# Kernel tuning notes

Measured on AMD Instinct MI355X. Metric: run time of the kernel, lower is better.

## Reference

```python
import jax, jax.numpy as jnp
import numpy as np

H = 8
D_MODEL = 512
D_K = D_MODEL // H
B = 8
S = 1024


def _linear(x, W, b):
    # torch nn.Linear: y = x @ W.T + b, W: [out, in]
    return jnp.einsum('bsd,ed->bse', x, W) + b


def _to_heads(x):
    # [B,S,D] -> [B,H,S,d_k]
    return x.reshape(B, S, H, D_K).transpose(0, 2, 1, 3)


def setup_inputs() -> dict:
    key = jax.random.key(0)
    ks = jax.random.split(key, 20)
    inp = {
        'input_rgb': jax.random.normal(ks[0], (B, S, D_MODEL), jnp.float32),
        'input_flow': jax.random.normal(ks[1], (B, S, D_MODEL), jnp.float32),
    }
    names = ['Wq1', 'Wk1', 'Wv1', 'Wq2', 'Wk2', 'Wv2', 'Wo1', 'Wo2']
    for i, n in enumerate(names):
        inp[n] = jax.random.normal(ks[2 + i], (D_MODEL, D_MODEL), jnp.float32) * 0.02
        inp['b' + n[1:]] = jax.random.normal(ks[10 + i], (D_MODEL,), jnp.float32) * 0.02
    return inp


def reference(input_rgb, input_flow, Wq1, bq1, Wk1, bk1, Wv1, bv1,
              Wq2, bq2, Wk2, bk2, Wv2, bv2, Wo1, bo1, Wo2, bo2):
    scale = 1.0 / jnp.sqrt(jnp.asarray(D_K, input_rgb.dtype))

    q_r = _to_heads(_linear(input_rgb, Wq1, bq1))
    k_r = _to_heads(_linear(input_rgb, Wk1, bk1))
    v_r = _to_heads(_linear(input_rgb, Wv1, bv1))
    q_f = _to_heads(_linear(input_flow, Wq2, bq2))
    k_f = _to_heads(_linear(input_flow, Wk2, bk2))
    v_f = _to_heads(_linear(input_flow, Wv2, bv2))

    # two full [B,H,S,S] softmax attention maps
    attn_rgb = jax.nn.softmax(jnp.einsum('bhqd,bhkd->bhqk', q_r, k_r) * scale, axis=-1)
    attn_flow = jax.nn.softmax(jnp.einsum('bhqd,bhkd->bhqk', q_f, k_f) * scale, axis=-1)
    # elementwise max merge (breaks flash-attention fusion)
    attn = jnp.maximum(attn_rgb, attn_flow)

    # Attention2: out = attn @ value (dropout is identity in eval mode)
    out_rgb = jnp.einsum('bhqk,bhkd->bhqd', attn, v_r)
    out_flow = jnp.einsum('bhqk,bhkd->bhqd', attn, v_f)

    out_rgb = out_rgb.transpose(0, 2, 1, 3).reshape(B, S, D_MODEL)
    out_flow = out_flow.transpose(0, 2, 1, 3).reshape(B, S, D_MODEL)
    return (_linear(out_rgb, Wo1, bo1), _linear(out_flow, Wo2, bo2))
```

## Files before the change

### kernel.cpp

```cpp
#include <hip/hip_runtime.h>
#include <hip/hip_bf16.h>


typedef unsigned short u16;
typedef __attribute__((ext_vector_type(8))) short short8;
typedef __attribute__((ext_vector_type(4))) short s4pack;
typedef __attribute__((ext_vector_type(4))) float floatx4;

#define B_DIM 8
#define S_DIM 1024
#define H_DIM 8
#define DK 64
#define DMODEL 512
#define NTOK (B_DIM * S_DIM)
#define SEG ((size_t)NTOK * DMODEL)
#define WSEG ((size_t)DMODEL * DMODEL)

#define SCHED_FENCE() __builtin_amdgcn_sched_barrier(0)
#define LGKM0() asm volatile("s_waitcnt lgkmcnt(0)" ::: "memory")
#define BARRIER() __builtin_amdgcn_s_barrier()

__device__ __forceinline__ floatx4 mfma_bf16(short8 a, short8 b, floatx4 c) {
  return __builtin_amdgcn_mfma_f32_16x16x32_bf16(a, b, c, 0, 0, 0);
}

__device__ __forceinline__ u16 f32_to_bf16_rne(float f) {
  unsigned u = __float_as_uint(f);
  unsigned r = u + 0x7FFFu + ((u >> 16) & 1u);
  return (u16)(r >> 16);
}

__device__ __forceinline__ float bf16_bits_to_f32(u16 u) {
  return __uint_as_float(((unsigned)u) << 16);
}

__device__ __forceinline__ void async_cp16(const u16* g, u16* lds) {
  __builtin_amdgcn_global_load_lds(
      (__attribute__((address_space(1))) void*)(const_cast<u16*>(g)),
      (__attribute__((address_space(3))) void*)(lds), 16, 0, 0);
}

#define NT_CONV 18
#define CCHUNK 8192
struct ConvParams {
  const void* src[NT_CONV];
  u16* dst[NT_CONV];
  int n[NT_CONV];
  int coff[NT_CONV + 1];
};

__global__ __launch_bounds__(256) void convert_inputs(ConvParams p) {
  __shared__ int flag_f32;
  const int blk = blockIdx.x;
  int t = 0;
  while (t + 1 < NT_CONV && blk >= p.coff[t + 1]) ++t;
  const int lc = blk - p.coff[t];
  const int n = p.n[t];
  const int tid = threadIdx.x;

  if (tid < 64) {
    const u16* s = (const u16*)p.src[t];
    int bad = 0;
#pragma unroll
    for (int j = 0; j < 8; ++j) {
      float f = bf16_bits_to_f32(s[tid * 8 + j]);
      bad |= !(fabsf(f) < 1e4f);
    }
    bad |= __shfl_xor(bad, 1);
    bad |= __shfl_xor(bad, 2);
    bad |= __shfl_xor(bad, 4);
    bad |= __shfl_xor(bad, 8);
    bad |= __shfl_xor(bad, 16);
    bad |= __shfl_xor(bad, 32);
    if (tid == 0) flag_f32 = bad;
  }
  __syncthreads();
  const int is_f32 = flag_f32;
  const int base = lc * CCHUNK;

#pragma unroll
  for (int it = 0; it < CCHUNK / 2048; ++it) {
    const int idx = base + (it * 256 + tid) * 8;
    if (idx + 8 > n) break;
    if (!is_f32) {
      *(short8*)&p.dst[t][idx] = *(const short8*)&((const u16*)p.src[t])[idx];
    } else {
      const float* s = (const float*)p.src[t] + idx;
      short8 o;
#pragma unroll
      for (int j = 0; j < 8; ++j) o[j] = (short)f32_to_bf16_rne(s[j]);
      *(short8*)&p.dst[t][idx] = o;
    }
  }
}

__device__ __forceinline__ void gemm128_mainloop(
    const u16* __restrict__ A, const u16* __restrict__ W,
    int m0, int n0, u16* ldsA, u16* ldsB, floatx4 acc[4][4]) {
  const int tid = threadIdx.x;
  const int lane = tid & 63;
  const int wid = tid >> 6;
  const int wm = wid >> 1, wn = wid & 1;
  const int r = lane & 15, g = lane >> 4;

  const int stg_row = wid * 32 + (lane >> 2);
  const int stg_col = (((lane & 3) ^ ((lane >> 3) & 3)) * 8);

  const u16* ga0 = A + (size_t)(m0 + stg_row) * DMODEL + stg_col;
  const u16* ga1 = A + (size_t)(m0 + stg_row + 16) * DMODEL + stg_col;
  const u16* gb0 = W + (size_t)(n0 + stg_row) * DMODEL + stg_col;
  const u16* gb1 = W + (size_t)(n0 + stg_row + 16) * DMODEL + stg_col;
  const int lo0 = (wid * 32) * 32;
  const int lo1 = (wid * 32 + 16) * 32;

#pragma unroll
  for (int t = 0; t < 3; ++t) {
    const int nb = t * 4096;
    const int ko = t * 32;
    async_cp16(ga0 + ko, ldsA + nb + lo0);
    async_cp16(ga1 + ko, ldsA + nb + lo1);
    async_cp16(gb0 + ko, ldsB + nb + lo0);
    async_cp16(gb1 + ko, ldsB + nb + lo1);
  }

  const int rc = ((g ^ ((r >> 1) & 3)) * 8);

#pragma unroll
  for (int kt = 0; kt < 16; ++kt) {
    SCHED_FENCE();
    if (kt < 14)       asm volatile("s_waitcnt vmcnt(8)" ::: "memory");
    else if (kt == 14) asm volatile("s_waitcnt vmcnt(4)" ::: "memory");
    else               asm volatile("s_waitcnt vmcnt(0)" ::: "memory");
    BARRIER();
    SCHED_FENCE();

    const int cb = (kt % 3) * 4096;
    short8 a[4], b[4];
#pragma unroll
    for (int i = 0; i < 4; ++i)
      a[i] = *(const short8*)&ldsA[cb + (wm * 64 + i * 16 + r) * 32 + rc];
#pragma unroll
    for (int j = 0; j < 4; ++j)
      b[j] = *(const short8*)&ldsB[cb + (wn * 64 + j * 16 + r) * 32 + rc];
#pragma unroll
    for (int i = 0; i < 4; ++i)
#pragma unroll
      for (int j = 0; j < 4; ++j)
        acc[i][j] = mfma_bf16(a[i], b[j], acc[i][j]);

    if (kt + 3 < 16) {
      SCHED_FENCE(); BARRIER(); SCHED_FENCE();
      const int ko = (kt + 3) * 32;
      async_cp16(ga0 + ko, ldsA + cb + lo0);
      async_cp16(ga1 + ko, ldsA + cb + lo1);
      async_cp16(gb0 + ko, ldsB + cb + lo0);
      async_cp16(gb1 + ko, ldsB + cb + lo1);
    }
  }
}

struct QkvParams {
  const u16* X[2];
  const u16* W[2][3];
  const u16* Bias[2][3];
  u16* Out[2][3];
};

__global__ __launch_bounds__(256) void qkv_gemm(QkvParams p) {
  __shared__ u16 ldsA[3 * 128 * 32];
  __shared__ u16 ldsB[3 * 128 * 32];
  const int lin = blockIdx.x;
  const int wg = (lin & 7) * 192 + (lin >> 3);
  const int m0 = (wg / 24) * 128;
  const int c = wg % 24;
  const int z = c / 12;
  const int yc = c % 12;
  const int wi = yc >> 2;
  const int n0 = (yc & 3) * 128;

  floatx4 acc[4][4];
  const floatx4 z4 = {0.f, 0.f, 0.f, 0.f};
#pragma unroll
  for (int i = 0; i < 4; ++i)
#pragma unroll
    for (int j = 0; j < 4; ++j) acc[i][j] = z4;

  gemm128_mainloop(p.X[z], p.W[z][wi], m0, n0, ldsA, ldsB, acc);

  const int tid = threadIdx.x, lane = tid & 63, wid = tid >> 6;
  const int wm = wid >> 1, wn = wid & 1, r = lane & 15, g = lane >> 4;
  const u16* bias = p.Bias[z][wi];
  u16* out = p.Out[z][wi];
  const float qscale = 0.125f * 1.4426950408889634f;

#pragma unroll
  for (int j = 0; j < 4; ++j) {
    const int cc = n0 + wn * 64 + j * 16 + r;
    const float bv = bf16_bits_to_f32(bias[cc]);
    const int h = cc >> 6, d = cc & 63;
#pragma unroll
    for (int i = 0; i < 4; ++i) {
      const int row0 = m0 + wm * 64 + i * 16 + g * 4;
      const int bb = row0 >> 10, ss0 = row0 & 1023;
      if (wi == 2) {
        s4pack pk;
#pragma unroll
        for (int ii = 0; ii < 4; ++ii)
          pk[ii] = (short)f32_to_bf16_rne(acc[i][j][ii] + bv);
        *(s4pack*)&out[(((size_t)(bb * H_DIM + h)) * DK + d) * S_DIM + ss0] = pk;
      } else {
#pragma unroll
        for (int ii = 0; ii < 4; ++ii) {
          float v = acc[i][j][ii] + bv;
          if (wi == 0) v *= qscale;
          out[(((size_t)(bb * H_DIM + h)) * S_DIM + (ss0 + ii)) * DK + d] =
              f32_to_bf16_rne(v);
        }
      }
    }
  }
}

#define KVB 64
#define QB 128

struct AttnParams {
  const u16* Q[2];
  const u16* K[2];
  const u16* Vt[2];
  u16* O[2];
};

__global__ __launch_bounds__(256, 2) void attn_merged(AttnParams p) {
  __shared__ u16 Ks[2][KVB * 64];
  __shared__ u16 Vs[2][64 * KVB];

  const int tid = threadIdx.x;
  const int lane = tid & 63;
  const int wid = tid >> 6;
  const int r = lane & 15, g = lane >> 4;

  const int lin = blockIdx.x;
  const int w = (lin & 7) * 64 + (lin >> 3);
  const int bh = w >> 3;
  const int q0 = (w & 7) * QB;
  const size_t hbase = (size_t)bh * S_DIM * DK;

  const int krow = tid >> 3, kch = tid & 7;
  const int sK = (krow & 3) | (((krow >> 3) & 1) << 2);
  const int kdst0 = krow * 64 + ((kch ^ sK) * 8);
  const int kdst1 = (krow + 32) * 64 + ((kch ^ sK) * 8);
  const size_t kg0 = (size_t)krow * DK + kch * 8;
  const size_t kg1 = kg0 + (size_t)32 * DK;

  const int vrow = tid >> 3, vch = tid & 7;
  const int sV = vrow & 7;
  const int vdst0 = vrow * KVB + ((vch ^ sV) * 8);
  const int vdst1 = (vrow + 32) * KVB + ((vch ^ sV) * 8);
  const size_t vg0 = (size_t)vrow * S_DIM + vch * 8;
  const size_t vg1 = vg0 + (size_t)32 * S_DIM;

  const int srg = (r & 3) | (((r >> 2) & 1) << 2);
  const int prow = ((r >> 2) * 8 + (r & 3)) * 64;
  const int cA0 = (g ^ srg) * 8;
  const int cA1 = ((4 + g) ^ srg) * 8;

  short8 qf[2][2][2];
#pragma unroll
  for (int s = 0; s < 2; ++s)
#pragma unroll
    for (int mt = 0; mt < 2; ++mt)
#pragma unroll
      for (int kc = 0; kc < 2; ++kc)
        qf[s][mt][kc] = *(const short8*)
            &p.Q[s][hbase + (size_t)(q0 + wid * 32 + mt * 16 + r) * DK +
                    kc * 32 + g * 8];

  short8 kst[2][2], vst[2][2];
#pragma unroll
  for (int s = 0; s < 2; ++s) {
    kst[s][0] = *(const short8*)&p.K[s][hbase + kg0];
    kst[s][1] = *(const short8*)&p.K[s][hbase + kg1];
  }

  const floatx4 z4 = {0.f, 0.f, 0.f, 0.f};
  float sl[2][2] = {{0.f, 0.f}, {0.f, 0.f}};

  for (int kt = 0; kt < 16; ++kt) {
    if (kt) { SCHED_FENCE(); BARRIER(); SCHED_FENCE(); }
#pragma unroll
    for (int s = 0; s < 2; ++s) {
      *(short8*)&Ks[s][kdst0] = kst[s][0];
      *(short8*)&Ks[s][kdst1] = kst[s][1];
    }
    if (kt < 15) {
      const size_t k0n = (size_t)(kt + 1) * KVB * DK;
#pragma unroll
      for (int s = 0; s < 2; ++s) {
        kst[s][0] = *(const short8*)&p.K[s][hbase + k0n + kg0];
        kst[s][1] = *(const short8*)&p.K[s][hbase + k0n + kg1];
      }
    }
    SCHED_FENCE(); LGKM0(); BARRIER(); SCHED_FENCE();

#pragma unroll
    for (int kb = 0; kb < 2; ++kb) {
      const int ro = kb * 2048 + prow;
#pragma unroll
      for (int s = 0; s < 2; ++s) {
        const short8 kA0 = *(const short8*)&Ks[s][ro + cA0];
        const short8 kA1 = *(const short8*)&Ks[s][ro + cA1];
        const short8 kB0 = *(const short8*)&Ks[s][ro + 256 + cA0];
        const short8 kB1 = *(const short8*)&Ks[s][ro + 256 + cA1];
#pragma unroll
        for (int mt = 0; mt < 2; ++mt) {
          floatx4 aA = mfma_bf16(kA0, qf[s][mt][0], z4);
          aA = mfma_bf16(kA1, qf[s][mt][1], aA);
          floatx4 aB = mfma_bf16(kB0, qf[s][mt][0], z4);
          aB = mfma_bf16(kB1, qf[s][mt][1], aB);
          sl[s][mt] += __builtin_amdgcn_exp2f(aA[0]) + __builtin_amdgcn_exp2f(aA[1]) +
                       __builtin_amdgcn_exp2f(aA[2]) + __builtin_amdgcn_exp2f(aA[3]) +
                       __builtin_amdgcn_exp2f(aB[0]) + __builtin_amdgcn_exp2f(aB[1]) +
                       __builtin_amdgcn_exp2f(aB[2]) + __builtin_amdgcn_exp2f(aB[3]);
        }
      }
    }
  }

#pragma unroll
  for (int s = 0; s < 2; ++s) {
    kst[s][0] = *(const short8*)&p.K[s][hbase + kg0];
    kst[s][1] = *(const short8*)&p.K[s][hbase + kg1];
    vst[s][0] = *(const short8*)&p.Vt[s][hbase + vg0];
    vst[s][1] = *(const short8*)&p.Vt[s][hbase + vg1];
  }

  float inv_[2][2];
#pragma unroll
  for (int s = 0; s < 2; ++s)
#pragma unroll
    for (int mt = 0; mt < 2; ++mt) {
      float v = sl[s][mt];
      v += __shfl_xor(v, 16);
      v += __shfl_xor(v, 32);
      inv_[s][mt] = 1.0f / v;
    }

  floatx4 o_[2][2][4];
#pragma unroll
  for (int s = 0; s < 2; ++s)
#pragma unroll
    for (int mt = 0; mt < 2; ++mt)
#pragma unroll
      for (int nt = 0; nt < 4; ++nt) o_[s][mt][nt] = z4;

  for (int kt = 0; kt < 16; ++kt) {
    SCHED_FENCE(); BARRIER(); SCHED_FENCE();
#pragma unroll
    for (int s = 0; s < 2; ++s) {
      *(short8*)&Ks[s][kdst0] = kst[s][0];
      *(short8*)&Ks[s][kdst1] = kst[s][1];
      *(short8*)&Vs[s][vdst0] = vst[s][0];
      *(short8*)&Vs[s][vdst1] = vst[s][1];
    }
    if (kt < 15) {
      const size_t knk = (size_t)(kt + 1) * KVB;
#pragma unroll
      for (int s = 0; s < 2; ++s) {
        kst[s][0] = *(const short8*)&p.K[s][hbase + knk * DK + kg0];
        kst[s][1] = *(const short8*)&p.K[s][hbase + knk * DK + kg1];
        vst[s][0] = *(const short8*)&p.Vt[s][hbase + vg0 + knk];
        vst[s][1] = *(const short8*)&p.Vt[s][hbase + vg1 + knk];
      }
    }
    SCHED_FENCE(); LGKM0(); BARRIER(); SCHED_FENCE();

#pragma unroll
    for (int kb = 0; kb < 2; ++kb) {
      const int ro = kb * 2048 + prow;
      short8 kA0[2], kA1[2], kB0[2], kB1[2];
#pragma unroll
      for (int s = 0; s < 2; ++s) {
        kA0[s] = *(const short8*)&Ks[s][ro + cA0];
        kA1[s] = *(const short8*)&Ks[s][ro + cA1];
        kB0[s] = *(const short8*)&Ks[s][ro + 256 + cA0];
        kB1[s] = *(const short8*)&Ks[s][ro + 256 + cA1];
      }

      short8 pA[2];
#pragma unroll
      for (int mt = 0; mt < 2; ++mt) {
        floatx4 arA = mfma_bf16(kA0[0], qf[0][mt][0], z4);
        arA = mfma_bf16(kA1[0], qf[0][mt][1], arA);
        floatx4 arB = mfma_bf16(kB0[0], qf[0][mt][0], z4);
        arB = mfma_bf16(kB1[0], qf[0][mt][1], arB);
        floatx4 afA = mfma_bf16(kA0[1], qf[1][mt][0], z4);
        afA = mfma_bf16(kA1[1], qf[1][mt][1], afA);
        floatx4 afB = mfma_bf16(kB0[1], qf[1][mt][0], z4);
        afB = mfma_bf16(kB1[1], qf[1][mt][1], afB);
#pragma unroll
        for (int i = 0; i < 4; ++i) {
          const float prA = __builtin_amdgcn_exp2f(arA[i]) * inv_[0][mt];
          const float pfA = __builtin_amdgcn_exp2f(afA[i]) * inv_[1][mt];
          pA[mt][i] = (short)f32_to_bf16_rne(fmaxf(prA, pfA));
          const float prB = __builtin_amdgcn_exp2f(arB[i]) * inv_[0][mt];
          const float pfB = __builtin_amdgcn_exp2f(afB[i]) * inv_[1][mt];
          pA[mt][4 + i] = (short)f32_to_bf16_rne(fmaxf(prB, pfB));
        }
      }

      short8 vB[2][4];
#pragma unroll
      for (int s = 0; s < 2; ++s)
#pragma unroll
        for (int nt = 0; nt < 4; ++nt)
          vB[s][nt] = *(const short8*)
              &Vs[s][(nt * 16 + r) * KVB + (((kb * 4 + g) ^ (r & 7)) * 8)];

#pragma unroll
      for (int s = 0; s < 2; ++s)
#pragma unroll
        for (int mt = 0; mt < 2; ++mt)
#pragma unroll
          for (int nt = 0; nt < 4; ++nt)
            o_[s][mt][nt] = mfma_bf16(pA[mt], vB[s][nt], o_[s][mt][nt]);
    }
  }

  const int bb = bh >> 3, h = bh & 7;
#pragma unroll
  for (int s = 0; s < 2; ++s) {
    u16* out = p.O[s];
#pragma unroll
    for (int mt = 0; mt < 2; ++mt)
#pragma unroll
      for (int nt = 0; nt < 4; ++nt) {
        const int col = h * 64 + nt * 16 + r;
#pragma unroll
        for (int i = 0; i < 4; ++i) {
          const int row = q0 + wid * 32 + mt * 16 + g * 4 + i;
          out[((size_t)bb * S_DIM + row) * DMODEL + col] =
              f32_to_bf16_rne(o_[s][mt][nt][i]);
        }
      }
  }
}

struct OutParams {
  const u16* A[2];
  const u16* W[2];
  const u16* Bias[2];
  float* Out[2];
};

__global__ __launch_bounds__(256) void out_gemm(OutParams p) {
  __shared__ u16 ldsA[3 * 128 * 32];
  __shared__ u16 ldsB[3 * 128 * 32];
  const int lin = blockIdx.x;
  const int wg = (lin & 7) * 64 + (lin >> 3);
  const int m0 = (wg >> 3) * 128;
  const int c = wg & 7;
  const int z = c >> 2;
  const int n0 = (c & 3) * 128;

  floatx4 acc[4][4];
  const floatx4 z4 = {0.f, 0.f, 0.f, 0.f};
#pragma unroll
  for (int i = 0; i < 4; ++i)
#pragma unroll
    for (int j = 0; j < 4; ++j) acc[i][j] = z4;

  gemm128_mainloop(p.A[z], p.W[z], m0, n0, ldsA, ldsB, acc);

  const int tid = threadIdx.x, lane = tid & 63, wid = tid >> 6;
  const int wm = wid >> 1, wn = wid & 1, r = lane & 15, g = lane >> 4;
  const u16* bias = p.Bias[z];
  float* out = p.Out[z];

#pragma unroll
  for (int j = 0; j < 4; ++j) {
    const int cc = n0 + wn * 64 + j * 16 + r;
    const float bv = bf16_bits_to_f32(bias[cc]);
#pragma unroll
    for (int i = 0; i < 4; ++i) {
      const int row0 = m0 + wm * 64 + i * 16 + g * 4;
#pragma unroll
      for (int ii = 0; ii < 4; ++ii)
        out[(size_t)(row0 + ii) * DMODEL + cc] = acc[i][j][ii] + bv;
    }
  }
}

extern "C" void kernel_launch(void* const* d_in, const int* in_sizes, int n_in,
                              void* d_out, int out_size, void* d_ws, size_t ws_size,
                              hipStream_t stream) {
  (void)in_sizes; (void)n_in; (void)out_size; (void)ws_size;
  u16* ws = (u16*)d_ws;
  u16* Qr = ws + 0 * SEG;
  u16* Kr = ws + 1 * SEG;
  u16* Vr = ws + 2 * SEG;
  u16* Qf = ws + 3 * SEG;
  u16* Kf = ws + 4 * SEG;
  u16* Vf = ws + 5 * SEG;
  u16* Or = ws + 6 * SEG;
  u16* Of = ws + 7 * SEG;
  u16* cW = ws + 8 * SEG;
  u16* cB = cW + 8 * WSEG;

  ConvParams cp;
  int coff = 0;
  for (int i = 0; i < NT_CONV; ++i) {
    cp.src[i] = d_in[i];
    int n;
    if (i < 2) {
      n = (int)SEG;
      cp.dst[i] = (i == 0) ? Or : Of;
    } else {
      const int k = (i - 2) >> 1;
      const int isb = (i - 2) & 1;
      n = isb ? DMODEL : (int)WSEG;
      cp.dst[i] = isb ? (cB + k * DMODEL) : (cW + k * WSEG);
    }
    cp.n[i] = n;
    cp.coff[i] = coff;
    coff += (n + CCHUNK - 1) / CCHUNK;
  }
  cp.coff[NT_CONV] = coff;
  convert_inputs<<<dim3(coff), dim3(256), 0, stream>>>(cp);

  QkvParams qp;
  qp.X[0] = Or;
  qp.X[1] = Of;
  for (int s = 0; s < 2; ++s)
    for (int wi = 0; wi < 3; ++wi) {
      const int k = s * 3 + wi;
      qp.W[s][wi] = cW + k * WSEG;
      qp.Bias[s][wi] = cB + k * DMODEL;
    }
  qp.Out[0][0] = Qr; qp.Out[0][1] = Kr; qp.Out[0][2] = Vr;
  qp.Out[1][0] = Qf; qp.Out[1][1] = Kf; qp.Out[1][2] = Vf;
  qkv_gemm<<<dim3(1536), dim3(256), 0, stream>>>(qp);

  AttnParams ap;
  ap.Q[0] = Qr; ap.Q[1] = Qf;
  ap.K[0] = Kr; ap.K[1] = Kf;
  ap.Vt[0] = Vr; ap.Vt[1] = Vf;
  ap.O[0] = Or; ap.O[1] = Of;
  attn_merged<<<dim3(512), dim3(256), 0, stream>>>(ap);

  OutParams op;
  op.A[0] = Or; op.A[1] = Of;
  op.W[0] = cW + 6 * WSEG; op.Bias[0] = cB + 6 * DMODEL;
  op.W[1] = cW + 7 * WSEG; op.Bias[1] = cB + 7 * DMODEL;
  op.Out[0] = (float*)d_out;
  op.Out[1] = (float*)d_out + SEG;
  out_gemm<<<dim3(512), dim3(256), 0, stream>>>(op);
}
```

Before: 232.5 us.

## Enlarge projection GEMM tiles to 256x256 with 512 threads and double buffering

Replaces the 128x128 GEMM mainloop, which used a triple-buffered 32-wide K pipeline, with a 256x256 tile per 512-thread block. It now double-buffers 64-wide K slices with a new XOR swizzle. The larger tile is meant to raise arithmetic intensity and cut global and LDS traffic per FLOP for the QKV and output projections. In exchange the grids shrink to 384 and 128 blocks on a GPU with many CUs, so occupancy and load balance may suffer, and register pressure rises with 32 accumulators per thread.

Measured after the change: 248.7 us. 7.0% more time.

```diff
diff --git a/kernel.cpp b/kernel.cpp
--- a/kernel.cpp
+++ b/kernel.cpp
@@ -94,69 +94,66 @@
   }
 }
 
-__device__ __forceinline__ void gemm128_mainloop(
+__device__ __forceinline__ void gemm256_mainloop(
     const u16* __restrict__ A, const u16* __restrict__ W,
-    int m0, int n0, u16* ldsA, u16* ldsB, floatx4 acc[4][4]) {
+    int m0, int n0, u16* ldsA, u16* ldsB, floatx4 acc[8][4]) {
   const int tid = threadIdx.x;
   const int lane = tid & 63;
   const int wid = tid >> 6;
-  const int wm = wid >> 1, wn = wid & 1;
+  const int wm = wid >> 2, wn = wid & 3;
   const int r = lane & 15, g = lane >> 4;
 
-  const int stg_row = wid * 32 + (lane >> 2);
-  const int stg_col = (((lane & 3) ^ ((lane >> 3) & 3)) * 8);
-
-  const u16* ga0 = A + (size_t)(m0 + stg_row) * DMODEL + stg_col;
-  const u16* ga1 = A + (size_t)(m0 + stg_row + 16) * DMODEL + stg_col;
-  const u16* gb0 = W + (size_t)(n0 + stg_row) * DMODEL + stg_col;
-  const u16* gb1 = W + (size_t)(n0 + stg_row + 16) * DMODEL + stg_col;
-  const int lo0 = (wid * 32) * 32;
-  const int lo1 = (wid * 32 + 16) * 32;
-
-#pragma unroll
-  for (int t = 0; t < 3; ++t) {
-    const int nb = t * 4096;
-    const int ko = t * 32;
-    async_cp16(ga0 + ko, ldsA + nb + lo0);
-    async_cp16(ga1 + ko, ldsA + nb + lo1);
-    async_cp16(gb0 + ko, ldsB + nb + lo0);
-    async_cp16(gb1 + ko, ldsB + nb + lo1);
-  }
-
-  const int rc = ((g ^ ((r >> 1) & 3)) * 8);
-
-#pragma unroll
-  for (int kt = 0; kt < 16; ++kt) {
+  const int srow = wid * 32 + (lane >> 3);
+  const int sch = ((lane & 7) ^ (srow & 7)) * 8;
+  const u16* gaS = A + (size_t)(m0 + srow) * DMODEL + sch;
+  const u16* gbS = W + (size_t)(n0 + srow) * DMODEL + sch;
+  const int ldst = (wid * 32) * 64;
+
+#define STAGE256(kt, buf)                                                  \
+  do {                                                                     \
+    const int _o = (buf) * 16384;                                          \
+    const size_t _k = (size_t)(kt) * 64;                                   \
+    _Pragma("unroll") for (int _t = 0; _t < 4; ++_t) {                     \
+      async_cp16(gaS + _k + _t * 8 * DMODEL, ldsA + _o + ldst + _t * 512); \
+      async_cp16(gbS + _k + _t * 8 * DMODEL, ldsB + _o + ldst + _t * 512); \
+    }                                                                      \
+  } while (0)
+
+  const int rc0 = ((g) ^ (r & 7)) * 8;
+  const int rc1 = ((4 + g) ^ (r & 7)) * 8;
+
+  STAGE256(0, 0);
+
+#pragma unroll
+  for (int kt = 0; kt < 8; ++kt) {
+    const int cur = kt & 1;
+    if (kt) { SCHED_FENCE(); BARRIER(); SCHED_FENCE(); }
+    if (kt < 7) STAGE256(kt + 1, cur ^ 1);
     SCHED_FENCE();
-    if (kt < 14)       asm volatile("s_waitcnt vmcnt(8)" ::: "memory");
-    else if (kt == 14) asm volatile("s_waitcnt vmcnt(4)" ::: "memory");
-    else               asm volatile("s_waitcnt vmcnt(0)" ::: "memory");
+    if (kt < 7) asm volatile("s_waitcnt vmcnt(8)" ::: "memory");
+    else        asm volatile("s_waitcnt vmcnt(0)" ::: "memory");
     BARRIER();
     SCHED_FENCE();
 
-    const int cb = (kt % 3) * 4096;
-    short8 a[4], b[4];
-#pragma unroll
-    for (int i = 0; i < 4; ++i)
-      a[i] = *(const short8*)&ldsA[cb + (wm * 64 + i * 16 + r) * 32 + rc];
-#pragma unroll
-    for (int j = 0; j < 4; ++j)
-      b[j] = *(const short8*)&ldsB[cb + (wn * 64 + j * 16 + r) * 32 + rc];
-#pragma unroll
-    for (int i = 0; i < 4; ++i)
+    const int cb = cur * 16384;
+#pragma unroll
+    for (int kk = 0; kk < 2; ++kk) {
+      const int rc = kk ? rc1 : rc0;
+      short8 a[8], b[4];
+#pragma unroll
+      for (int i = 0; i < 8; ++i)
+        a[i] = *(const short8*)&ldsA[cb + (wm * 128 + i * 16 + r) * 64 + rc];
 #pragma unroll
       for (int j = 0; j < 4; ++j)
-        acc[i][j] = mfma_bf16(a[i], b[j], acc[i][j]);
-
-    if (kt + 3 < 16) {
-      SCHED_FENCE(); BARRIER(); SCHED_FENCE();
-      const int ko = (kt + 3) * 32;
-      async_cp16(ga0 + ko, ldsA + cb + lo0);
-      async_cp16(ga1 + ko, ldsA + cb + lo1);
-      async_cp16(gb0 + ko, ldsB + cb + lo0);
-      async_cp16(gb1 + ko, ldsB + cb + lo1);
-    }
-  }
+        b[j] = *(const short8*)&ldsB[cb + (wn * 64 + j * 16 + r) * 64 + rc];
+#pragma unroll
+      for (int i = 0; i < 8; ++i)
+#pragma unroll
+        for (int j = 0; j < 4; ++j)
+          acc[i][j] = mfma_bf16(a[i], b[j], acc[i][j]);
+    }
+  }
+#undef STAGE256
 }
 
 struct QkvParams {
@@ -166,29 +163,28 @@
   u16* Out[2][3];
 };
 
-__global__ __launch_bounds__(256) void qkv_gemm(QkvParams p) {
-  __shared__ u16 ldsA[3 * 128 * 32];
-  __shared__ u16 ldsB[3 * 128 * 32];
+__global__ __launch_bounds__(512, 1) void qkv_gemm(QkvParams p) {
+  __shared__ u16 ldsA[2 * 256 * 64];
+  __shared__ u16 ldsB[2 * 256 * 64];
   const int lin = blockIdx.x;
-  const int wg = (lin & 7) * 192 + (lin >> 3);
-  const int m0 = (wg / 24) * 128;
-  const int c = wg % 24;
-  const int z = c / 12;
-  const int yc = c % 12;
-  const int wi = yc >> 2;
-  const int n0 = (yc & 3) * 128;
-
-  floatx4 acc[4][4];
+  const int wg = (lin & 7) * 48 + (lin >> 3);
+  const int m0 = (wg / 12) * 256;
+  const int c = wg % 12;
+  const int z = c / 6;
+  const int wi = (c % 6) >> 1;
+  const int n0 = (c & 1) * 256;
+
+  floatx4 acc[8][4];
   const floatx4 z4 = {0.f, 0.f, 0.f, 0.f};
 #pragma unroll
-  for (int i = 0; i < 4; ++i)
+  for (int i = 0; i < 8; ++i)
 #pragma unroll
     for (int j = 0; j < 4; ++j) acc[i][j] = z4;
 
-  gemm128_mainloop(p.X[z], p.W[z][wi], m0, n0, ldsA, ldsB, acc);
+  gemm256_mainloop(p.X[z], p.W[z][wi], m0, n0, ldsA, ldsB, acc);
 
   const int tid = threadIdx.x, lane = tid & 63, wid = tid >> 6;
-  const int wm = wid >> 1, wn = wid & 1, r = lane & 15, g = lane >> 4;
+  const int wm = wid >> 2, wn = wid & 3, r = lane & 15, g = lane >> 4;
   const u16* bias = p.Bias[z][wi];
   u16* out = p.Out[z][wi];
   const float qscale = 0.125f * 1.4426950408889634f;
@@ -199,8 +195,8 @@
     const float bv = bf16_bits_to_f32(bias[cc]);
     const int h = cc >> 6, d = cc & 63;
 #pragma unroll
-    for (int i = 0; i < 4; ++i) {
-      const int row0 = m0 + wm * 64 + i * 16 + g * 4;
+    for (int i = 0; i < 8; ++i) {
+      const int row0 = m0 + wm * 128 + i * 16 + g * 4;
       const int bb = row0 >> 10, ss0 = row0 & 1023;
       if (wi == 2) {
         s4pack pk;
@@ -453,27 +449,27 @@
   float* Out[2];
 };
 
-__global__ __launch_bounds__(256) void out_gemm(OutParams p) {
-  __shared__ u16 ldsA[3 * 128 * 32];
-  __shared__ u16 ldsB[3 * 128 * 32];
+__global__ __launch_bounds__(512, 1) void out_gemm(OutParams p) {
+  __shared__ u16 ldsA[2 * 256 * 64];
+  __shared__ u16 ldsB[2 * 256 * 64];
   const int lin = blockIdx.x;
-  const int wg = (lin & 7) * 64 + (lin >> 3);
-  const int m0 = (wg >> 3) * 128;
-  const int c = wg & 7;
-  const int z = c >> 2;
-  const int n0 = (c & 3) * 128;
-
-  floatx4 acc[4][4];
+  const int wg = (lin & 7) * 16 + (lin >> 3);
+  const int m0 = (wg >> 2) * 256;
+  const int c = wg & 3;
+  const int z = c >> 1;
+  const int n0 = (c & 1) * 256;
+
+  floatx4 acc[8][4];
   const floatx4 z4 = {0.f, 0.f, 0.f, 0.f};
 #pragma unroll
-  for (int i = 0; i < 4; ++i)
+  for (int i = 0; i < 8; ++i)
 #pragma unroll
     for (int j = 0; j < 4; ++j) acc[i][j] = z4;
 
-  gemm128_mainloop(p.A[z], p.W[z], m0, n0, ldsA, ldsB, acc);
+  gemm256_mainloop(p.A[z], p.W[z], m0, n0, ldsA, ldsB, acc);
 
   const int tid = threadIdx.x, lane = tid & 63, wid = tid >> 6;
-  const int wm = wid >> 1, wn = wid & 1, r = lane & 15, g = lane >> 4;
+  const int wm = wid >> 2, wn = wid & 3, r = lane & 15, g = lane >> 4;
   const u16* bias = p.Bias[z];
   float* out = p.Out[z];
 
@@ -482,8 +478,8 @@
     const int cc = n0 + wn * 64 + j * 16 + r;
     const float bv = bf16_bits_to_f32(bias[cc]);
 #pragma unroll
-    for (int i = 0; i < 4; ++i) {
-      const int row0 = m0 + wm * 64 + i * 16 + g * 4;
+    for (int i = 0; i < 8; ++i) {
+      const int row0 = m0 + wm * 128 + i * 16 + g * 4;
 #pragma unroll
       for (int ii = 0; ii < 4; ++ii)
         out[(size_t)(row0 + ii) * DMODEL + cc] = acc[i][j][ii] + bv;
@@ -539,7 +535,7 @@
     }
   qp.Out[0][0] = Qr; qp.Out[0][1] = Kr; qp.Out[0][2] = Vr;
   qp.Out[1][0] = Qf; qp.Out[1][1] = Kf; qp.Out[1][2] = Vf;
-  qkv_gemm<<<dim3(1536), dim3(256), 0, stream>>>(qp);
+  qkv_gemm<<<dim3(384), dim3(512), 0, stream>>>(qp);
 
   AttnParams ap;
   ap.Q[0] = Qr; ap.Q[1] = Qf;
@@ -554,5 +550,5 @@
   op.W[1] = cW + 7 * WSEG; op.Bias[1] = cB + 7 * DMODEL;
   op.Out[0] = (float*)d_out;
   op.Out[1] = (float*)d_out + SEG;
-  out_gemm<<<dim3(512), dim3(256), 0, stream>>>(op);
-}
+  out_gemm<<<dim3(128), dim3(512), 0, stream>>>(op);
+}
```
